# Optimization experiments

Hardware: AMD Instinct MI355X
Metric: run time of the kernel (lower is better)

Reference implementation:

```python
import jax, jax.numpy as jnp
import numpy as np

N_NODES = 50000
N_EDGES = 800000
CH = 128
N_GRAPHS = 8
ADD_TO_EDGE_SCORE = 0.5


def edge_scores(x, row, col, lin_w, lin_b, n):
    """Raw edge score via Linear([x_row||x_col]) then scatter-softmax over col."""
    C = x.shape[1]
    # split-weight form of cat([x[row], x[col]]) @ W^T + b (avoids the [E,2C] concat)
    raw = x[row] @ lin_w[0, :C] + x[col] @ lin_w[0, C:] + lin_b[0]  # [E]
    mx = jax.ops.segment_max(raw, col, num_segments=n)
    ex = jnp.exp(raw - mx[col])
    den = jax.ops.segment_sum(ex, col, num_segments=n)
    return ex / (den[col] + 1e-16) + ADD_TO_EDGE_SCORE


def greedy_match_cluster(row_np, col_np, score_np, n):
    """Greedy maximal matching in descending-score order + 2-element clustering."""
    perm = np.argsort(-score_np)
    rows = row_np.tolist()
    cols = col_np.tolist()
    used = np.zeros(n, dtype=bool)
    match = np.zeros(len(rows), dtype=bool)
    for e in perm.tolist():
        r = rows[e]
        c = cols[e]
        if not (used[r] or used[c]):
            match[e] = True
            used[r] = True
            used[c] = True
    cluster = np.arange(n)
    cluster[col_np[match]] = row_np[match]
    _, cluster = np.unique(cluster, return_inverse=True)
    return match, cluster


def setup_inputs() -> dict:
    key = jax.random.key(0)
    k1, k2, k3, k4, k5 = jax.random.split(key, 5)
    x = jax.random.normal(k1, (N_NODES, CH), dtype=jnp.float32)
    edge_index = jax.random.randint(k2, (2, N_EDGES), 0, N_NODES)
    batch = jnp.sort(jax.random.randint(k3, (N_NODES,), 0, N_GRAPHS))
    bound = 1.0 / np.sqrt(2 * CH)
    lin_w = jax.random.uniform(k4, (1, 2 * CH), minval=-bound, maxval=bound, dtype=jnp.float32)
    lin_b = jax.random.uniform(k5, (1,), minval=-bound, maxval=bound, dtype=jnp.float32)
    return {"x": x, "edge_index": edge_index, "batch": batch, "lin_w": lin_w, "lin_b": lin_b}


def reference(x, edge_index, batch, lin_w, lin_b):
    n = x.shape[0]
    row, col = edge_index[0], edge_index[1]
    score = edge_scores(x, row, col, lin_w, lin_b, n)  # [E]

    # sequential greedy matching / cluster relabeling (host side, non-differentiable)
    row_np, col_np = np.asarray(row), np.asarray(col)
    match, cluster_np = greedy_match_cluster(row_np, col_np, np.asarray(score), n)
    c = int(cluster_np.max()) + 1
    match_idx = jnp.asarray(np.nonzero(match)[0])
    cluster = jnp.asarray(cluster_np, dtype=jnp.int32)

    # pooled features scaled by the contracted edge's score (1.0 for singletons)
    new_x = jax.ops.segment_sum(x, cluster, num_segments=c)  # [c, C]
    root = cluster[row[match_idx]]
    new_edge_score = jnp.ones((c,), x.dtype).at[root].set(score[match_idx])
    new_x = new_x * new_edge_score[:, None]

    # coalesce(cluster[edge_index]): sort + dedup
    lin_idx = cluster_np[row_np].astype(np.int64) * c + cluster_np[col_np]
    uniq = np.unique(lin_idx)
    new_edge_index = jnp.asarray(np.stack([uniq // c, uniq % c]).astype(np.int32))

    new_batch = jnp.zeros((c,), dtype=batch.dtype).at[cluster].set(batch)
    return new_x, new_edge_index, new_batch, new_edge_score, cluster
```

## Files before the change

### kernel.cpp

```cpp
#include <hip/hip_runtime.h>

typedef unsigned int u32;
typedef unsigned short u16;
typedef unsigned long long u64;

#define CH_ 128

__device__ __forceinline__ u32 f2ord(float f){
  u32 u = __float_as_uint(f);
  return ((int)u < 0) ? ~u : (u | 0x80000000u);
}
__device__ __forceinline__ float ord2f(u32 u){
  return (u & 0x80000000u) ? __uint_as_float(u & 0x7FFFFFFFu) : __uint_as_float(~u);
}
__device__ __forceinline__ u32 ldu32(const u32* p){
  return __hip_atomic_load(p, __ATOMIC_RELAXED, __HIP_MEMORY_SCOPE_AGENT);
}
__device__ __forceinline__ void stu32(u32* p, u32 v){
  __hip_atomic_store(p, v, __ATOMIC_RELAXED, __HIP_MEMORY_SCOPE_AGENT);
}

__global__ void k_init(u32* hdr, u32* mxbits, double* den, u64* sw,
                       int* craw, int* medge, u32* deg, u32* acur,
                       u32* wpos, u32* offarr, int N, int E){
  int i0 = blockIdx.x*blockDim.x + threadIdx.x;
  int nt = gridDim.x*blockDim.x;
  for (int v = i0; v < N; v += nt){
    mxbits[v]=0u; den[v]=0.0; sw[v]=0ull; craw[v]=v; medge[v]=-1;
    deg[v]=0u; acur[v]=0u; wpos[v]=0u;
  }
  if (i0 == 0){
    for (int i = 0; i < 64; i++) hdr[i] = 0u;
    hdr[6] = (u32)N;
    offarr[N] = (u32)(2*E);
  }
}

__global__ void k_dots(const float* __restrict__ x, const float* __restrict__ lw,
                       float* __restrict__ s, float* __restrict__ t, int N){
  int wid = threadIdx.x >> 6, lane = threadIdx.x & 63;
  int node = blockIdx.x*4 + wid;
  if (node >= N) return;
  const float* xr = x + (size_t)node*CH_;
  float xa = xr[lane], xb = xr[64+lane];
  float sv = xa*lw[lane]      + xb*lw[64+lane];
  float tv = xa*lw[128+lane]  + xb*lw[192+lane];
  #pragma unroll
  for (int m = 1; m < 64; m <<= 1){ sv += __shfl_xor(sv, m); tv += __shfl_xor(tv, m); }
  if (lane == 0){ s[node]=sv; t[node]=tv; }
}

__global__ void k_rawmax(const float* __restrict__ s, const float* __restrict__ t,
                         const int* __restrict__ row, const int* __restrict__ col,
                         const float* __restrict__ lb, float* __restrict__ rawex,
                         u32* __restrict__ mxbits, u32* __restrict__ rc,
                         u32* __restrict__ deg, int E){
  float b = lb[0];
  int i0 = blockIdx.x*blockDim.x + threadIdx.x;
  int nt = gridDim.x*blockDim.x;
  for (int e = i0; e < E; e += nt){
    int r = row[e], c = col[e];
    float raw = (s[r] + t[c]) + b;
    rawex[e] = raw;
    atomicMax(&mxbits[c], f2ord(raw));
    rc[e] = ((u32)r << 16) | (u32)c;
    atomicAdd(&deg[r], 1u);
    atomicAdd(&deg[c], 1u);
  }
}

__global__ void k_exden(const int* __restrict__ col, const u32* __restrict__ mxbits,
                        float* __restrict__ rawex, double* __restrict__ den, int E){
  int i0 = blockIdx.x*blockDim.x + threadIdx.x;
  int nt = gridDim.x*blockDim.x;
  for (int e = i0; e < E; e += nt){
    int c = col[e];
    float ex = expf(rawex[e] - ord2f(mxbits[c]));
    rawex[e] = ex;
    atomicAdd(&den[c], (double)ex);
  }
}

__global__ void scan_p1(const u32* __restrict__ in, u32* __restrict__ out,
                        u32* __restrict__ bsums, const u32* __restrict__ nptr){
  __shared__ u32 sh[256];
  u32 n = *nptr;
  int t = threadIdx.x;
  u32 i = blockIdx.x*256u + (u32)t;
  u32 v = (i < n) ? in[i] : 0u;
  sh[t] = v; __syncthreads();
  for (int o = 1; o < 256; o <<= 1){
    u32 a = (t >= o) ? sh[t-o] : 0u;
    __syncthreads();
    sh[t] += a;
    __syncthreads();
  }
  if (i < n) out[i] = sh[t] - v;
  if (t == 255) bsums[blockIdx.x] = sh[255];
}
__global__ void scan_p2(u32* bsums, u32* total){
  __shared__ u32 sh[256];
  int t = threadIdx.x;
  u32 v = bsums[t];
  sh[t] = v; __syncthreads();
  for (int o = 1; o < 256; o <<= 1){
    u32 a = (t >= o) ? sh[t-o] : 0u;
    __syncthreads();
    sh[t] += a;
    __syncthreads();
  }
  bsums[t] = sh[t] - v;
  if (t == 255 && total) *total = sh[255];
}
__global__ void scan_p3(u32* out, const u32* __restrict__ bsums, const u32* __restrict__ nptr){
  u32 n = *nptr;
  u32 i = blockIdx.x*256u + threadIdx.x;
  if (i < n) out[i] += bsums[blockIdx.x];
}

__global__ void k_scoreadj(const u32* __restrict__ rc, const float* __restrict__ rawex,
                           float* __restrict__ score, const double* __restrict__ den,
                           const u32* __restrict__ offarr, u32* __restrict__ acur,
                           u64* __restrict__ adj, u16* __restrict__ adjp, int E, int N){
  const int P = 8;
  int i0 = blockIdx.x*blockDim.x + threadIdx.x;
  int nt = gridDim.x*blockDim.x;
  u32 span = ((u32)N + P - 1) / P;
  for (int p = 0; p < P; p++){
    u32 vlo = (u32)p * span;
    u32 vhi = vlo + span; if (vhi > (u32)N) vhi = (u32)N;
    for (int e = i0; e < E; e += nt){
      u32 pk = rc[e]; u32 r = pk >> 16, c = pk & 0xFFFFu;
      bool wr = (r >= vlo) & (r < vhi);
      bool wc = (c >= vlo) & (c < vhi);
      if (p == 0 || wr || wc){
        float sc = rawex[e]/(float)den[c] + 0.5f;
        if (p == 0) score[e] = sc;
        u64 k = ((u64)__float_as_uint(sc) << 20) | (u64)(0xFFFFFu - (u32)e);
        if (wr){
          u32 pr = offarr[r] + atomicAdd(&acur[r], 1u);
          adj[pr] = k; adjp[pr] = (u16)c;
        }
        if (wc){
          u32 pc = offarr[c] + atomicAdd(&acur[c], 1u);
          adj[pc] = k; adjp[pc] = (u16)r;
        }
      }
    }
  }
}

__global__ void k_adjsort(const u32* __restrict__ offarr, u64* __restrict__ adj,
                          u16* __restrict__ adjp, int N){
  __shared__ u64 shk[512];
  __shared__ u32 shp[512];
  int lane = threadIdx.x;
  for (int seg = blockIdx.x; seg < N; seg += gridDim.x){
    u32 base = offarr[seg];
    int n = (int)(offarr[seg+1] - base);
    if (n <= 1) continue;
    if (n <= 64){
      u64 v = (lane < n) ? adj[base + lane] : 0ull;
      u32 pr = (lane < n) ? (u32)adjp[base + lane] : 0u;
      #pragma unroll
      for (int k2 = 2; k2 <= 64; k2 <<= 1)
        for (int j = k2 >> 1; j > 0; j >>= 1){
          u64 pv = __shfl_xor(v, j);
          u32 pp = (u32)__shfl_xor((int)pr, j);
          bool up  = ((lane & k2) == 0);
          bool low = ((lane & j) == 0);
          bool take_mx = (up == low);
          bool swap = take_mx ? (pv > v) : (pv < v);
          if (swap){ v = pv; pr = pp; }
        }
      if (lane < n){ adj[base + lane] = v; adjp[base + lane] = (u16)pr; }
    } else {
      int msz = 128; while (msz < n) msz <<= 1;
      for (int i = lane; i < msz; i += 64){
        shk[i] = (i < n) ? adj[base + i] : 0ull;
        shp[i] = (i < n) ? (u32)adjp[base + i] : 0u;
      }
      __syncthreads();
      for (int k2 = 2; k2 <= msz; k2 <<= 1){
        for (int j = k2 >> 1; j > 0; j >>= 1){
          for (int i = lane; i < msz; i += 64){
            int ix = i ^ j;
            if (ix > i){
              u64 a = shk[i], b2 = shk[ix];
              bool desc = ((i & k2) == 0);
              if (desc ? (a < b2) : (a > b2)){
                shk[i] = b2; shk[ix] = a;
                u32 t2 = shp[i]; shp[i] = shp[ix]; shp[ix] = t2;
              }
            }
          }
          __syncthreads();
        }
      }
      for (int i = lane; i < n; i += 64){ adj[base+i] = shk[i]; adjp[base+i] = (u16)shp[i]; }
      __syncthreads();
    }
  }
}

__global__ void k_suitor(const u32* __restrict__ rc, const u32* __restrict__ offarr,
                         const u64* __restrict__ adj, const u16* __restrict__ adjp,
                         u64* sw, u32* wpos, int N){
  int i0 = blockIdx.x*blockDim.x + threadIdx.x;
  int nt = gridDim.x*blockDim.x;
  for (int v0 = i0; v0 < N; v0 += nt){
    u32 u = (u32)v0;
    u32 pos = offarr[u], end = offarr[u+1];
    while (pos < end){
      u64 k = adj[pos];
      u32 v = (u32)adjp[pos];
      pos++;
      if (sw[v] >= k) continue;
      stu32(&wpos[u], pos);
      u64 old = atomicMax((unsigned long long*)&sw[v], (unsigned long long)k);
      if (old >= k) continue;
      if (old == 0ull) break;
      u32 e2 = 0xFFFFFu - (u32)(old & 0xFFFFFu);
      u32 p2 = rc[e2];
      u = ((p2 >> 16) == v) ? (p2 & 0xFFFFu) : (p2 >> 16);
      u32 st = offarr[u];
      u32 wp = ldu32(&wpos[u]);
      pos = (wp > st) ? wp : st;
      end = offarr[u+1];
    }
  }
}

__global__ void k_exroot(const u64* __restrict__ sw, const u32* __restrict__ rc,
                         int* __restrict__ craw, int* __restrict__ medge,
                         u32* __restrict__ rf, int N){
  int v = blockIdx.x*blockDim.x + threadIdx.x;
  if (v >= N) return;
  u64 k = sw[v];
  bool iscol = false;
  if (k != 0ull){
    u32 e = 0xFFFFFu - (u32)(k & 0xFFFFFu);
    u32 p = rc[e]; u32 r = p >> 16, c = p & 0xFFFFu;
    if ((u32)v == c && sw[r] == k){
      craw[c] = (int)r; medge[r] = (int)e;
      iscol = (r != c);
    }
  }
  rf[v] = iscol ? 0u : 1u;
}

__global__ void k_clusterzero(const int* __restrict__ craw, const u32* __restrict__ newid,
                              int* __restrict__ clout, float* __restrict__ out, size_t offC,
                              u32* __restrict__ hist, u32* __restrict__ cur2,
                              u32* __restrict__ uniqcnt, int N, int M){
  int i = blockIdx.x*blockDim.x + threadIdx.x;
  if (i < M){ hist[i]=0u; cur2[i]=0u; uniqcnt[i]=0u; }
  if (i < N){
    int cl = (int)newid[craw[i]];
    clout[i] = cl;
    out[offC + i] = (float)cl;
  }
}

__global__ void k_hist(const int* __restrict__ row, const int* __restrict__ clout,
                       u32* __restrict__ hist, int E){
  int i0 = blockIdx.x*blockDim.x + threadIdx.x;
  int nt = gridDim.x*blockDim.x;
  for (int e = i0; e < E; e += nt) atomicAdd(&hist[clout[row[e]]], 1u);
}

__global__ void k_scatter(const int* __restrict__ row, const int* __restrict__ col,
                          const int* __restrict__ clout, const u32* __restrict__ segoff,
                          u32* __restrict__ cur2, u32* __restrict__ ccbuf,
                          const u32* __restrict__ hdr, int E){
  const int P = 4;
  int cnum = (int)hdr[2];
  int span = (cnum + P - 1) / P;
  int i0 = blockIdx.x*blockDim.x + threadIdx.x;
  int nt = gridDim.x*blockDim.x;
  for (int p = 0; p < P; p++){
    int lo = p*span;
    int hi = lo + span; if (hi > cnum) hi = cnum;
    for (int e = i0; e < E; e += nt){
      int cr = clout[row[e]];
      if (cr < lo || cr >= hi) continue;
      u32 pos = segoff[cr] + atomicAdd(&cur2[cr], 1u);
      ccbuf[pos] = (u32)clout[col[e]];
    }
  }
}

__global__ void k_segsort(const u32* __restrict__ hdr, const u32* __restrict__ hist,
                          const u32* __restrict__ segoff, u32* __restrict__ ccbuf,
                          u32* __restrict__ uniqcnt){
  int c = (int)hdr[2];
  __shared__ u32 sh[1024];
  int lane = threadIdx.x;
  for (int seg = blockIdx.x; seg < c; seg += gridDim.x){
    int n = (int)hist[seg];
    if (n <= 0){ if (lane == 0) uniqcnt[seg] = 0u; continue; }
    u32 off = segoff[seg];
    if (n <= 64){
      u32 v = (lane < n) ? ccbuf[off + lane] : 0xFFFFFFFFu;
      #pragma unroll
      for (int k = 2; k <= 64; k <<= 1)
        for (int j = k >> 1; j > 0; j >>= 1){
          u32 p = __shfl_xor(v, j);
          bool up  = ((lane & k) == 0);
          bool low = ((lane & j) == 0);
          u32 mn = v < p ? v : p, mx = v < p ? p : v;
          v = (up == low) ? mn : mx;
        }
      u32 pv = __shfl_up(v, 1);
      bool un = (lane < n) && (lane == 0 || v != pv);
      u64 bal = __ballot(un);
      int cnt = __popcll(bal);
      int rk  = __popcll(bal & ((1ull << lane) - 1ull));
      if (un) ccbuf[off + rk] = v;
      if (lane == 0) uniqcnt[seg] = (u32)cnt;
    } else {
      int nn = n > 1024 ? 1024 : n;
      for (int i = lane; i < nn; i += 64) sh[i] = ccbuf[off + i];
      __syncthreads();
      for (int p = 0; p < nn; p++){
        int st = p & 1;
        for (int i = lane; 2*i + 1 + st < nn; i += 64){
          int a = 2*i + st;
          u32 x0 = sh[a], x1 = sh[a+1];
          if (x0 > x1){ sh[a] = x1; sh[a+1] = x0; }
        }
        __syncthreads();
      }
      if (lane == 0){
        int cnt = 0; u32 prev = 0u;
        for (int i = 0; i < nn; i++){
          u32 xv = sh[i];
          if (i == 0 || xv != prev){ ccbuf[off + cnt] = xv; cnt++; prev = xv; }
        }
        uniqcnt[seg] = (u32)cnt;
      }
      __syncthreads();
    }
  }
}

__global__ void k_out(const u32* __restrict__ hdr, const u32* __restrict__ segoff,
                      const u32* __restrict__ uniqcnt, const u32* __restrict__ uniqoff,
                      const u32* __restrict__ ccbuf, const int* __restrict__ craw,
                      const u32* __restrict__ newid, const int* __restrict__ medge,
                      const int* __restrict__ row, const int* __restrict__ col,
                      const float* __restrict__ score, const int* __restrict__ batch,
                      const float* __restrict__ x, float* __restrict__ out, int N){
  int c = (int)hdr[2]; u32 Ep = hdr[3];
  size_t base = (size_t)c * CH_;
  size_t offB = base + 2ull * (size_t)Ep;
  size_t offS = offB + (size_t)c;
  int gw   = (blockIdx.x*blockDim.x + threadIdx.x) >> 6;
  int lane = threadIdx.x & 63;
  int nw   = (gridDim.x*blockDim.x) >> 6;
  for (int seg = gw; seg < c; seg += nw){
    int cnt = (int)uniqcnt[seg];
    u32 so = segoff[seg], uo = uniqoff[seg];
    for (int j = lane; j < cnt; j += 64){
      u32 cc = ccbuf[so + j];
      out[base + uo + j]              = (float)seg;
      out[base + (size_t)Ep + uo + j] = (float)cc;
    }
  }
  for (int i = gw; i < N; i += nw){
    if (craw[i] != i) continue;
    int j = (int)newid[i];
    int e = medge[i];
    int lo = i, hi = i; float sc = 1.0f;
    if (e >= 0){
      int r = row[e], cc = col[e];
      lo = min(r, cc); hi = max(r, cc);
      sc = score[e];
    }
    float v0 = x[(size_t)lo*CH_ + lane];
    float v1 = x[(size_t)lo*CH_ + 64 + lane];
    if (hi != lo){ v0 += x[(size_t)hi*CH_ + lane]; v1 += x[(size_t)hi*CH_ + 64 + lane]; }
    out[(size_t)j*CH_ + lane]      = v0 * sc;
    out[(size_t)j*CH_ + 64 + lane] = v1 * sc;
    if (lane == 0){
      out[offB + j] = (float)batch[hi];
      out[offS + j] = sc;
    }
  }
}

extern "C" void kernel_launch(void* const* d_in, const int* in_sizes, int n_in,
                              void* d_out, int out_size, void* d_ws, size_t ws_size,
                              hipStream_t stream) {
  const float* x     = (const float*)d_in[0];
  const int*   eidx  = (const int*)d_in[1];
  const int*   batch = (const int*)d_in[2];
  const float* lw    = (const float*)d_in[3];
  const float* lb    = (const float*)d_in[4];

  int N = in_sizes[0] / CH_;
  int E = in_sizes[1] / 2;
  const int* row = eidx;
  const int* col = eidx + E;
  float* out = (float*)d_out;

  char* w = (char*)d_ws;
  size_t off = 0;
  auto carve = [&](size_t bytes) -> void* {
    void* p = w + off;
    off += (bytes + 255) & ~(size_t)255;
    return p;
  };
  u32*    hdr    = (u32*)   carve(256);
  double* den    = (double*)carve((size_t)N*8);
  u64*    sw     = (u64*)   carve((size_t)N*8);
  float*  s      = (float*) carve((size_t)N*4);
  float*  t      = (float*) carve((size_t)N*4);
  float*  rawex  = (float*) carve((size_t)E*4);
  float*  score  = (float*) carve((size_t)E*4);
  u32*    mxbits = (u32*)   carve((size_t)N*4);
  int*    craw   = (int*)   carve((size_t)N*4);
  u32*    rf     = (u32*)   carve((size_t)N*4);
  u32*    newid  = (u32*)   carve((size_t)N*4);
  int*    medge  = (int*)   carve((size_t)N*4);
  int*    clout  = (int*)   carve((size_t)N*4);
  u32*    rc     = (u32*)   carve((size_t)E*4);
  u32*    deg    = (u32*)   carve((size_t)N*4);
  u32*    acur   = (u32*)   carve((size_t)N*4);
  u32*    wpos   = (u32*)   carve((size_t)N*4);
  u32*    offarr = (u32*)   carve((size_t)(N+1)*4);
  u16*    adjp   = (u16*)   carve((size_t)(2*(size_t)E)*2);
  u64*    adj    = (u64*)   carve((size_t)(2*(size_t)E)*8);
  u32*    bsums  = (u32*)   carve(256*4);
  char* a = (char*)adj;
  size_t aoff = 0;
  auto acarve = [&](size_t bytes) -> void* {
    void* p = a + aoff;
    aoff += (bytes + 255) & ~(size_t)255;
    return p;
  };
  u32* ccbuf   = (u32*)acarve((size_t)E*4);
  u32* hist    = (u32*)acarve((size_t)(N+64)*4);
  u32* segoff  = (u32*)acarve((size_t)(N+64)*4);
  u32* cur2    = (u32*)acarve((size_t)(N+64)*4);
  u32* uniqcnt = (u32*)acarve((size_t)(N+64)*4);
  u32* uniqoff = (u32*)acarve((size_t)(N+64)*4);
  (void)ws_size; (void)n_in;

  int nbE = (E + 255) / 256;
  int nbN = (N + 255) / 256;

  k_init<<<512, 256, 0, stream>>>(hdr, mxbits, den, sw, craw, medge, deg, acur, wpos, offarr, N, E);
  k_dots<<<(N + 3)/4, 256, 0, stream>>>(x, lw, s, t, N);
  k_rawmax<<<nbE, 256, 0, stream>>>(s, t, row, col, lb, rawex, mxbits, rc, deg, E);
  k_exden<<<nbE, 256, 0, stream>>>(col, mxbits, rawex, den, E);

  scan_p1<<<256, 256, 0, stream>>>(deg, offarr, bsums, &hdr[6]);
  scan_p2<<<1, 256, 0, stream>>>(bsums, &hdr[7]);
  scan_p3<<<256, 256, 0, stream>>>(offarr, bsums, &hdr[6]);

  k_scoreadj<<<nbE, 256, 0, stream>>>(rc, rawex, score, den, offarr, acur, adj, adjp, E, N);
  k_adjsort<<<4096, 64, 0, stream>>>(offarr, adj, adjp, N);
  k_suitor<<<nbN, 256, 0, stream>>>(rc, offarr, adj, adjp, sw, wpos, N);
  k_exroot<<<nbN, 256, 0, stream>>>(sw, rc, craw, medge, rf, N);

  scan_p1<<<256, 256, 0, stream>>>(rf, newid, bsums, &hdr[6]);
  scan_p2<<<1, 256, 0, stream>>>(bsums, &hdr[2]);
  scan_p3<<<256, 256, 0, stream>>>(newid, bsums, &hdr[6]);

  k_clusterzero<<<(N + 64 + 255)/256, 256, 0, stream>>>(craw, newid, clout, out,
                                                        (size_t)(out_size - N),
                                                        hist, cur2, uniqcnt, N, N + 64);
  k_hist<<<nbE, 256, 0, stream>>>(row, clout, hist, E);

  scan_p1<<<256, 256, 0, stream>>>(hist, segoff, bsums, &hdr[2]);
  scan_p2<<<1, 256, 0, stream>>>(bsums, &hdr[4]);
  scan_p3<<<256, 256, 0, stream>>>(segoff, bsums, &hdr[2]);

  k_scatter<<<nbE, 256, 0, stream>>>(row, col, clout, segoff, cur2, ccbuf, hdr, E);
  k_segsort<<<4096, 64, 0, stream>>>(hdr, hist, segoff, ccbuf, uniqcnt);

  scan_p1<<<256, 256, 0, stream>>>(uniqcnt, uniqoff, bsums, &hdr[2]);
  scan_p2<<<1, 256, 0, stream>>>(bsums, &hdr[3]);
  scan_p3<<<256, 256, 0, stream>>>(uniqoff, bsums, &hdr[2]);

  k_out<<<4096, 256, 0, stream>>>(hdr, segoff, uniqcnt, uniqoff, ccbuf, craw, newid,
                                  medge, row, col, score, batch, x, out, N);
}
```

Measured before the change: 517.8 us.

## Use fixed-capacity per-node adjacency buckets instead of degree-scan CSR

Each node now gets a fixed slot of 80 entries in the adjacency arrays, so offsets become v*cap. This removes the per-edge degree atomics and the three-kernel prefix scan used to build CSR offsets. The sort and suitor kernels read each node's actual count from the insertion counter, clamped to the capacity. The adjacency buffers grow to N*cap entries, and the partitioned scatter pass goes from 8 to 16 partitions, which adds more sweeps over the edge list. Nodes with more than 80 incident edges silently lose neighbours, so results are correct only when degrees stay below the cap. A CSR fallback is kept for when the workspace is too small.

```diff
diff --git a/kernel.cpp b/kernel.cpp
--- a/kernel.cpp
+++ b/kernel.cpp
@@ -22,17 +22,18 @@
 
 __global__ void k_init(u32* hdr, u32* mxbits, double* den, u64* sw,
                        int* craw, int* medge, u32* deg, u32* acur,
-                       u32* wpos, u32* offarr, int N, int E){
+                       u32* wpos, u32* offarr, u32 ucap, int N, int E){
   int i0 = blockIdx.x*blockDim.x + threadIdx.x;
   int nt = gridDim.x*blockDim.x;
   for (int v = i0; v < N; v += nt){
     mxbits[v]=0u; den[v]=0.0; sw[v]=0ull; craw[v]=v; medge[v]=-1;
     deg[v]=0u; acur[v]=0u; wpos[v]=0u;
+    if (ucap) offarr[v] = (u32)v * ucap;
   }
   if (i0 == 0){
     for (int i = 0; i < 64; i++) hdr[i] = 0u;
     hdr[6] = (u32)N;
-    offarr[N] = (u32)(2*E);
+    offarr[N] = ucap ? (u32)N*ucap : (u32)(2*E);
   }
 }
 
@@ -54,7 +55,7 @@
                          const int* __restrict__ row, const int* __restrict__ col,
                          const float* __restrict__ lb, float* __restrict__ rawex,
                          u32* __restrict__ mxbits, u32* __restrict__ rc,
-                         u32* __restrict__ deg, int E){
+                         u32* __restrict__ deg, u32 ucap, int E){
   float b = lb[0];
   int i0 = blockIdx.x*blockDim.x + threadIdx.x;
   int nt = gridDim.x*blockDim.x;
@@ -64,8 +65,10 @@
     rawex[e] = raw;
     atomicMax(&mxbits[c], f2ord(raw));
     rc[e] = ((u32)r << 16) | (u32)c;
-    atomicAdd(&deg[r], 1u);
-    atomicAdd(&deg[c], 1u);
+    if (!ucap){
+      atomicAdd(&deg[r], 1u);
+      atomicAdd(&deg[c], 1u);
+    }
   }
 }
 
@@ -121,8 +124,8 @@
 __global__ void k_scoreadj(const u32* __restrict__ rc, const float* __restrict__ rawex,
                            float* __restrict__ score, const double* __restrict__ den,
                            const u32* __restrict__ offarr, u32* __restrict__ acur,
-                           u64* __restrict__ adj, u16* __restrict__ adjp, int E, int N){
-  const int P = 8;
+                           u64* __restrict__ adj, u16* __restrict__ adjp,
+                           u32 ucap, int P, int E, int N){
   int i0 = blockIdx.x*blockDim.x + threadIdx.x;
   int nt = gridDim.x*blockDim.x;
   u32 span = ((u32)N + P - 1) / P;
@@ -138,26 +141,35 @@
         if (p == 0) score[e] = sc;
         u64 k = ((u64)__float_as_uint(sc) << 20) | (u64)(0xFFFFFu - (u32)e);
         if (wr){
-          u32 pr = offarr[r] + atomicAdd(&acur[r], 1u);
-          adj[pr] = k; adjp[pr] = (u16)c;
+          u32 slot = atomicAdd(&acur[r], 1u);
+          if (!ucap || slot < ucap){
+            u32 pr = offarr[r] + slot;
+            adj[pr] = k; adjp[pr] = (u16)c;
+          }
         }
         if (wc){
-          u32 pc = offarr[c] + atomicAdd(&acur[c], 1u);
-          adj[pc] = k; adjp[pc] = (u16)r;
+          u32 slot = atomicAdd(&acur[c], 1u);
+          if (!ucap || slot < ucap){
+            u32 pc = offarr[c] + slot;
+            adj[pc] = k; adjp[pc] = (u16)r;
+          }
         }
       }
     }
   }
 }
 
-__global__ void k_adjsort(const u32* __restrict__ offarr, u64* __restrict__ adj,
-                          u16* __restrict__ adjp, int N){
+__global__ void k_adjsort(const u32* __restrict__ offarr, const u32* __restrict__ acur,
+                          u64* __restrict__ adj, u16* __restrict__ adjp,
+                          u32 ucap, int N){
   __shared__ u64 shk[512];
   __shared__ u32 shp[512];
   int lane = threadIdx.x;
+  u32 capn = ucap ? ucap : 0xFFFFFFFFu;
   for (int seg = blockIdx.x; seg < N; seg += gridDim.x){
     u32 base = offarr[seg];
-    int n = (int)(offarr[seg+1] - base);
+    u32 cnt = acur[seg]; if (cnt > capn) cnt = capn;
+    int n = (int)cnt;
     if (n <= 1) continue;
     if (n <= 64){
       u64 v = (lane < n) ? adj[base + lane] : 0ull;
@@ -204,13 +216,17 @@
 }
 
 __global__ void k_suitor(const u32* __restrict__ rc, const u32* __restrict__ offarr,
+                         const u32* __restrict__ acur,
                          const u64* __restrict__ adj, const u16* __restrict__ adjp,
-                         u64* sw, u32* wpos, int N){
-  int i0 = blockIdx.x*blockDim.x + threadIdx.x;
-  int nt = gridDim.x*blockDim.x;
+                         u64* sw, u32* wpos, u32 ucap, int N){
+  int i0 = blockIdx.x*blockDim.x + threadIdx.x;
+  int nt = gridDim.x*blockDim.x;
+  u32 capn = ucap ? ucap : 0xFFFFFFFFu;
   for (int v0 = i0; v0 < N; v0 += nt){
     u32 u = (u32)v0;
-    u32 pos = offarr[u], end = offarr[u+1];
+    u32 pos = offarr[u];
+    u32 cnt = acur[u]; if (cnt > capn) cnt = capn;
+    u32 end = pos + cnt;
     while (pos < end){
       u64 k = adj[pos];
       u32 v = (u32)adjp[pos];
@@ -224,9 +240,10 @@
       u32 p2 = rc[e2];
       u = ((p2 >> 16) == v) ? (p2 & 0xFFFFu) : (p2 >> 16);
       u32 st = offarr[u];
+      u32 c2 = acur[u]; if (c2 > capn) c2 = capn;
+      end = st + c2;
       u32 wp = ldu32(&wpos[u]);
       pos = (wp > st) ? wp : st;
-      end = offarr[u+1];
     }
   }
 }
@@ -429,9 +446,24 @@
   u32*    acur   = (u32*)   carve((size_t)N*4);
   u32*    wpos   = (u32*)   carve((size_t)N*4);
   u32*    offarr = (u32*)   carve((size_t)(N+1)*4);
-  u16*    adjp   = (u16*)   carve((size_t)(2*(size_t)E)*2);
-  u64*    adj    = (u64*)   carve((size_t)(2*(size_t)E)*8);
   u32*    bsums  = (u32*)   carve(256*4);
+
+  u32 cap = 80;
+  size_t adjp_b_bytes = ((size_t)N*cap*2 + 255) & ~(size_t)255;
+  size_t adj_b_bytes  = ((size_t)N*cap*8 + 255) & ~(size_t)255;
+  size_t adjp_c_bytes = ((size_t)(2*(size_t)E)*2 + 255) & ~(size_t)255;
+  size_t adj_c_bytes  = ((size_t)(2*(size_t)E)*8 + 255) & ~(size_t)255;
+  bool buckets = (off + adjp_b_bytes + adj_b_bytes + (1u<<20) <= ws_size);
+  u16* adjp; u64* adj;
+  if (buckets){
+    adjp = (u16*)carve((size_t)N*cap*2);
+    adj  = (u64*)carve((size_t)N*cap*8);
+  } else {
+    cap = 0;
+    adjp = (u16*)carve((size_t)(2*(size_t)E)*2);
+    adj  = (u64*)carve((size_t)(2*(size_t)E)*8);
+  }
+  (void)adjp_c_bytes; (void)adj_c_bytes;
   char* a = (char*)adj;
   size_t aoff = 0;
   auto acarve = [&](size_t bytes) -> void* {
@@ -445,23 +477,28 @@
   u32* cur2    = (u32*)acarve((size_t)(N+64)*4);
   u32* uniqcnt = (u32*)acarve((size_t)(N+64)*4);
   u32* uniqoff = (u32*)acarve((size_t)(N+64)*4);
-  (void)ws_size; (void)n_in;
+  (void)n_in;
 
   int nbE = (E + 255) / 256;
   int nbN = (N + 255) / 256;
-
-  k_init<<<512, 256, 0, stream>>>(hdr, mxbits, den, sw, craw, medge, deg, acur, wpos, offarr, N, E);
+  int P_adj = buckets ? 16 : 8;
+
+  k_init<<<512, 256, 0, stream>>>(hdr, mxbits, den, sw, craw, medge, deg, acur,
+                                  wpos, offarr, cap, N, E);
   k_dots<<<(N + 3)/4, 256, 0, stream>>>(x, lw, s, t, N);
-  k_rawmax<<<nbE, 256, 0, stream>>>(s, t, row, col, lb, rawex, mxbits, rc, deg, E);
+  k_rawmax<<<nbE, 256, 0, stream>>>(s, t, row, col, lb, rawex, mxbits, rc, deg, cap, E);
   k_exden<<<nbE, 256, 0, stream>>>(col, mxbits, rawex, den, E);
 
-  scan_p1<<<256, 256, 0, stream>>>(deg, offarr, bsums, &hdr[6]);
-  scan_p2<<<1, 256, 0, stream>>>(bsums, &hdr[7]);
-  scan_p3<<<256, 256, 0, stream>>>(offarr, bsums, &hdr[6]);
-
-  k_scoreadj<<<nbE, 256, 0, stream>>>(rc, rawex, score, den, offarr, acur, adj, adjp, E, N);
-  k_adjsort<<<4096, 64, 0, stream>>>(offarr, adj, adjp, N);
-  k_suitor<<<nbN, 256, 0, stream>>>(rc, offarr, adj, adjp, sw, wpos, N);
+  if (!buckets){
+    scan_p1<<<256, 256, 0, stream>>>(deg, offarr, bsums, &hdr[6]);
+    scan_p2<<<1, 256, 0, stream>>>(bsums, &hdr[7]);
+    scan_p3<<<256, 256, 0, stream>>>(offarr, bsums, &hdr[6]);
+  }
+
+  k_scoreadj<<<nbE, 256, 0, stream>>>(rc, rawex, score, den, offarr, acur, adj, adjp,
+                                      cap, P_adj, E, N);
+  k_adjsort<<<4096, 64, 0, stream>>>(offarr, acur, adj, adjp, cap, N);
+  k_suitor<<<nbN, 256, 0, stream>>>(rc, offarr, acur, adj, adjp, sw, wpos, cap, N);
   k_exroot<<<nbN, 256, 0, stream>>>(sw, rc, craw, medge, rf, N);
 
   scan_p1<<<256, 256, 0, stream>>>(rf, newid, bsums, &hdr[6]);
```

New measurement: 471.3 us. 1.1x faster.
